# Kernel optimization log

Measured on AMD Instinct MI355X. Metric: run time of the kernel, lower is better.

The kernel has to match this reference:

```python
import jax, jax.numpy as jnp
import numpy as np

B, C, T, F = 4, 2, 4224, 256
L = 256          # sequence_len (block size over time)
STRIDE = 128
H = 8            # num_heads
RF = L // 2      # receptive_field default


def setup_inputs() -> dict:
    key = jax.random.key(0)
    k0, k1, k2, k3, k4 = jax.random.split(key, 5)
    s = 0.05
    return {
        "x": jax.random.normal(k0, (B, C, T, F), dtype=jnp.float32),
        "w_in": jax.random.normal(k1, (3 * F, F), dtype=jnp.float32) * s,
        "b_in": jax.random.normal(k2, (3 * F,), dtype=jnp.float32) * s,
        "w_out": jax.random.normal(k3, (F, F), dtype=jnp.float32) * s,
        "b_out": jax.random.normal(k4, (F,), dtype=jnp.float32) * s,
    }


def reference(x, w_in, b_in, w_out, b_out):
    b, c, t, f = x.shape
    nb = (t - L) // STRIDE + 1              # num_blocks
    dh = f // H                              # head dim

    # --- UnfoldSpectrogram: (B,C,T,F) -> (B,C,nb,L,F) ---
    idx = jnp.arange(nb)[:, None] * STRIDE + jnp.arange(L)[None, :]  # (nb, L)
    blocks = x[:, :, idx, :]                 # (B,C,nb,L,F)

    # --- MultiheadAttention over flattened batch of blocks ---
    xb = blocks.reshape(b * c * nb, L, f)    # (N,L,F)
    qkv = xb @ w_in.T + b_in                 # (N,L,3F)
    q, k, v = jnp.split(qkv, 3, axis=-1)
    q = q.reshape(-1, L, H, dh)
    k = k.reshape(-1, L, H, dh)
    v = v.reshape(-1, L, H, dh)

    scale = 1.0 / np.sqrt(dh).astype(np.float32)
    scores = jnp.einsum("nihd,njhd->nhij", q, k) * scale  # (N,H,L,L)

    # Faithful to the original: the Longformer mask is a FLOAT 0/1 tensor that
    # torch's MultiheadAttention ADDS to the scores (band gets +1.0).
    di = jnp.arange(L)[:, None] - jnp.arange(L)[None, :]
    band = ((di >= 0) & (di < RF)).astype(scores.dtype)   # (L,L)
    scores = scores + band

    attn = jax.nn.softmax(scores, axis=-1)
    o = jnp.einsum("nhij,njhd->nihd", attn, v).reshape(-1, L, f)
    o = o @ w_out.T + b_out                  # (N,L,F)

    # --- FoldSpectrogram: overlap-add then normalize by overlap count ---
    ob = o.reshape(b, c, nb, L, f)
    y = jnp.zeros((b, c, t, f), dtype=o.dtype).at[:, :, idx, :].add(ob)
    cnt = jnp.zeros((t,), dtype=o.dtype).at[idx.reshape(-1)].add(1.0)
    return y / cnt[None, None, :, None]
```

## Files before the change

### kernel.cpp

```cpp
#include <hip/hip_runtime.h>

typedef unsigned short u16;
typedef unsigned int u32;
typedef __attribute__((ext_vector_type(8))) short bf16x8;
typedef __attribute__((ext_vector_type(4))) float f32x4;
typedef __attribute__((ext_vector_type(4))) u32 u32x4;
typedef __attribute__((ext_vector_type(2))) u32 u32x2;

__device__ __forceinline__ u16 f2bf(float f) {
  u32 u = __builtin_bit_cast(u32, f);
  return (u16)((u + 0x7FFFu + ((u >> 16) & 1u)) >> 16);
}
__device__ __forceinline__ float bf2f(u16 b) {
  return __builtin_bit_cast(float, (u32)b << 16);
}

__device__ __forceinline__ float fexp2(float x) {
#if __has_builtin(__builtin_amdgcn_exp2f)
  return __builtin_amdgcn_exp2f(x);
#else
  return __expf(x * 0.6931471805599453f);
#endif
}

__device__ __forceinline__ void lds_async16(const void* g, void* l) {
  auto gp = reinterpret_cast<const __attribute__((address_space(1))) u32*>(
      reinterpret_cast<uintptr_t>(g));
  auto lp = reinterpret_cast<__attribute__((address_space(3))) u32*>(
      reinterpret_cast<uintptr_t>(l));
  __builtin_amdgcn_global_load_lds(gp, lp, 16, 0, 0);
}

__global__ void cvt_kernel(const float* __restrict__ in, u16* __restrict__ out, int n4) {
  int i = blockIdx.x * 256 + threadIdx.x;
  if (i < n4) {
    f32x4 v = *(const f32x4*)(in + (size_t)i * 4);
    u32x2 o;
    o[0] = (u32)f2bf(v[0]) | ((u32)f2bf(v[1]) << 16);
    o[1] = (u32)f2bf(v[2]) | ((u32)f2bf(v[3]) << 16);
    *(u32x2*)(out + (size_t)i * 4) = o;
  }
}

__global__ void cvt2_kernel(const float* __restrict__ a, const float* __restrict__ b,
                            u16* __restrict__ oa, u16* __restrict__ ob, int na4, int nb4) {
  int i = blockIdx.x * 256 + threadIdx.x;
  const float* src;
  u16* dst;
  int idx;
  if (i < na4) {
    src = a; dst = oa; idx = i;
  } else {
    idx = i - na4;
    if (idx >= nb4) return;
    src = b; dst = ob;
  }
  f32x4 v = *(const f32x4*)(src + (size_t)idx * 4);
  u32x2 o;
  o[0] = (u32)f2bf(v[0]) | ((u32)f2bf(v[1]) << 16);
  o[1] = (u32)f2bf(v[2]) | ((u32)f2bf(v[3]) << 16);
  *(u32x2*)(dst + (size_t)idx * 4) = o;
}

template <bool OUT_BF16>
__global__ __launch_bounds__(256) void gemm_bt_kernel(
    const u16* __restrict__ A, const u16* __restrict__ B,
    const float* __restrict__ bias, void* __restrict__ C,
    int M, int N, int K) {
  __shared__ u16 sA[128 * 32];
  __shared__ u16 sB[128 * 32];
  const int tid = threadIdx.x;
  const int m0 = blockIdx.x * 128;
  const int n0 = blockIdx.y * 128;
  const int w = tid >> 6;
  const int lane = tid & 63;
  const int wr = (w >> 1) * 64;
  const int wc = (w & 1) * 64;
  const int lm = lane & 15;
  const int lk = (lane >> 4) * 8;

  f32x4 acc[4][4] = {};

  const int srow = tid >> 2;
  const int ssub = (tid & 3) * 8;
  const u16* Ag = A + (size_t)(m0 + srow) * K + ssub;
  const u16* Bg = B + (size_t)(n0 + srow) * K + ssub;
  const size_t rstep = (size_t)64 * K;

  for (int k0 = 0; k0 < K; k0 += 32) {
    __syncthreads();
    lds_async16(Ag + k0, &sA[tid * 8]);
    lds_async16(Ag + rstep + k0, &sA[2048 + tid * 8]);
    lds_async16(Bg + k0, &sB[tid * 8]);
    lds_async16(Bg + rstep + k0, &sB[2048 + tid * 8]);
    __syncthreads();
    bf16x8 af[4], bfr[4];
#pragma unroll
    for (int i = 0; i < 4; ++i)
      af[i] = *(const bf16x8*)&sA[(wr + i * 16 + lm) * 32 + lk];
#pragma unroll
    for (int j = 0; j < 4; ++j)
      bfr[j] = *(const bf16x8*)&sB[(wc + j * 16 + lm) * 32 + lk];
#pragma unroll
    for (int i = 0; i < 4; ++i)
#pragma unroll
      for (int j = 0; j < 4; ++j)
        acc[i][j] = __builtin_amdgcn_mfma_f32_16x16x32_bf16(af[i], bfr[j], acc[i][j], 0, 0, 0);
  }

  const int r0 = (lane >> 4) * 4;
#pragma unroll
  for (int j = 0; j < 4; ++j) {
    const int n = n0 + wc + j * 16 + lm;
    const float bv = bias[n];
#pragma unroll
    for (int i = 0; i < 4; ++i) {
#pragma unroll
      for (int r = 0; r < 4; ++r) {
        const int m = m0 + wr + i * 16 + r0 + r;
        float v = acc[i][j][r] + bv;
        if (OUT_BF16)
          ((u16*)C)[(size_t)m * N + n] = f2bf(v);
        else
          ((float*)C)[(size_t)m * N + n] = v;
      }
    }
  }
}

__global__ __launch_bounds__(256, 2) void attn_kernel(const u16* __restrict__ qkv,
                                                      u16* __restrict__ o_ws) {
  __shared__ u16 sVt[32 * 264];
  __shared__ u16 sP[4 * 32 * 40];

  const int bid = blockIdx.x;
  const int n = bid >> 3;
  const int h = bid & 7;
  const int rowbase = (n >> 5) * 4224 + (n & 31) * 128;
  const int tid = threadIdx.x;
  const int w = tid >> 6;
  const int lane = tid & 63;
  const int lm = lane & 15;
  const int lg = lane >> 4;

#pragma unroll
  for (int it = 0; it < 4; ++it) {
    int c = it * 256 + tid;
    int row = c >> 2;
    int sub = (c & 3) * 8;
    const u16* gv = qkv + (size_t)(rowbase + row) * 768 + 512 + h * 32 + sub;
    u32x4 vv = *(const u32x4*)gv;
#pragma unroll
    for (int q = 0; q < 4; ++q) {
      sVt[(sub + 2 * q) * 264 + row] = (u16)(vv[q] & 0xFFFFu);
      sVt[(sub + 2 * q + 1) * 264 + row] = (u16)(vv[q] >> 16);
    }
  }

  bf16x8 qf[4];
#pragma unroll
  for (int rt = 0; rt < 4; ++rt) {
    int row = rowbase + w * 64 + rt * 16 + lm;
    qf[rt] = *(const bf16x8*)(qkv + (size_t)row * 768 + h * 32 + lg * 8);
  }

  __syncthreads();

  f32x4 oacc[4][2] = {};
  float lsum[4] = {0.f, 0.f, 0.f, 0.f};
  u16* myP = sP + w * (32 * 40);
  const float C1 = 0.25500035370494726f;
  const float C2 = 1.4426950408889634f;
  const int jq = lg * 4;
  const u16* kbase = qkv + (size_t)(rowbase + lm) * 768 + 256 + h * 32 + lg * 8;
  const int D0w = w * 64;

#pragma unroll 1
  for (int ch = 0; ch < 8; ++ch) {
    bf16x8 kf[2], vf[2];
#pragma unroll
    for (int ct = 0; ct < 2; ++ct)
      kf[ct] = *(const bf16x8*)(kbase + (size_t)(ch * 32 + ct * 16) * 768);
#pragma unroll
    for (int ctd = 0; ctd < 2; ++ctd)
      vf[ctd] = *(const bf16x8*)&sVt[(ctd * 16 + lm) * 264 + ch * 32 + lg * 8];

#pragma unroll
    for (int hf = 0; hf < 2; ++hf) {
#pragma unroll
      for (int ct = 0; ct < 2; ++ct) {
#pragma unroll
        for (int rl = 0; rl < 2; ++rl) {
          const int rt = hf * 2 + rl;
          f32x4 s = __builtin_amdgcn_mfma_f32_16x16x32_bf16(kf[ct], qf[rt], f32x4{0.f, 0.f, 0.f, 0.f}, 0, 0, 0);
          const int D0 = D0w + rt * 16 - (ch * 32 + ct * 16);
          float p0, p1, p2, p3;
          if (D0 >= 16 && D0 <= 112) {
            p0 = fexp2(__builtin_fmaf(s[0], C1, C2));
            p1 = fexp2(__builtin_fmaf(s[1], C1, C2));
            p2 = fexp2(__builtin_fmaf(s[2], C1, C2));
            p3 = fexp2(__builtin_fmaf(s[3], C1, C2));
          } else if (D0 == 0) {
            p0 = fexp2(__builtin_fmaf(s[0], C1, (lm >= jq + 0) ? C2 : 0.0f));
            p1 = fexp2(__builtin_fmaf(s[1], C1, (lm >= jq + 1) ? C2 : 0.0f));
            p2 = fexp2(__builtin_fmaf(s[2], C1, (lm >= jq + 2) ? C2 : 0.0f));
            p3 = fexp2(__builtin_fmaf(s[3], C1, (lm >= jq + 3) ? C2 : 0.0f));
          } else if (D0 == 128) {
            p0 = fexp2(__builtin_fmaf(s[0], C1, (lm < jq + 0) ? C2 : 0.0f));
            p1 = fexp2(__builtin_fmaf(s[1], C1, (lm < jq + 1) ? C2 : 0.0f));
            p2 = fexp2(__builtin_fmaf(s[2], C1, (lm < jq + 2) ? C2 : 0.0f));
            p3 = fexp2(__builtin_fmaf(s[3], C1, (lm < jq + 3) ? C2 : 0.0f));
          } else {
            p0 = fexp2(s[0] * C1);
            p1 = fexp2(s[1] * C1);
            p2 = fexp2(s[2] * C1);
            p3 = fexp2(s[3] * C1);
          }
          lsum[rt] += (p0 + p1) + (p2 + p3);
          u32 u0 = __builtin_bit_cast(u32, p0) + 0x8000u;
          u32 u1 = __builtin_bit_cast(u32, p1) + 0x8000u;
          u32 u2 = __builtin_bit_cast(u32, p2) + 0x8000u;
          u32 u3 = __builtin_bit_cast(u32, p3) + 0x8000u;
          u32x2 pk;
          pk[0] = __builtin_amdgcn_perm(u1, u0, 0x07060302u);
          pk[1] = __builtin_amdgcn_perm(u3, u2, 0x07060302u);
          *(u32x2*)&myP[(rl * 16 + lm) * 40 + ct * 16 + jq] = pk;
        }
      }
      bf16x8 pf[2];
#pragma unroll
      for (int rl = 0; rl < 2; ++rl)
        pf[rl] = *(const bf16x8*)&myP[(rl * 16 + lm) * 40 + lg * 8];
      __asm__ __volatile__("" ::: "memory");
#pragma unroll
      for (int rl = 0; rl < 2; ++rl)
#pragma unroll
        for (int ctd = 0; ctd < 2; ++ctd)
          oacc[hf * 2 + rl][ctd] =
              __builtin_amdgcn_mfma_f32_16x16x32_bf16(pf[rl], vf[ctd], oacc[hf * 2 + rl][ctd], 0, 0, 0);
    }
  }

  float linv[4];
#pragma unroll
  for (int rt = 0; rt < 4; ++rt) {
    float v = lsum[rt];
    v += __shfl_xor(v, 16);
    v += __shfl_xor(v, 32);
    linv[rt] = 1.0f / v;
  }

#pragma unroll
  for (int rt = 0; rt < 4; ++rt) {
#pragma unroll
    for (int r = 0; r < 4; ++r) {
      float inv = __shfl(linv[rt], jq + r);
      int i_g = w * 64 + rt * 16 + jq + r;
#pragma unroll
      for (int ctd = 0; ctd < 2; ++ctd) {
        float v = oacc[rt][ctd][r] * inv;
        u32 u = __builtin_bit_cast(u32, v) + 0x8000u;
        o_ws[((size_t)(n * 256 + i_g)) * 256 + h * 32 + ctd * 16 + lm] = (u16)(u >> 16);
      }
    }
  }
}

__global__ void combine_kernel(const u16* __restrict__ o_ws, u16* __restrict__ oc) {
  int gid = blockIdx.x * 256 + threadIdx.x;
  int m = gid >> 5;
  int f0 = (gid & 31) << 3;
  int bc = m / 4224;
  int t = m - bc * 4224;
  int i0 = t >> 7;
  float a[8] = {0.f, 0.f, 0.f, 0.f, 0.f, 0.f, 0.f, 0.f};
  if (i0 <= 31) {
    const u16* p = o_ws + ((size_t)((bc * 32 + i0) * 256 + (t - (i0 << 7)))) * 256 + f0;
    u32x4 v = *(const u32x4*)p;
#pragma unroll
    for (int q = 0; q < 4; ++q) {
      a[2 * q] += bf2f((u16)(v[q] & 0xFFFFu));
      a[2 * q + 1] += bf2f((u16)(v[q] >> 16));
    }
  }
  if (i0 >= 1) {
    int i1 = i0 - 1;
    const u16* p = o_ws + ((size_t)((bc * 32 + i1) * 256 + (t - (i1 << 7)))) * 256 + f0;
    u32x4 v = *(const u32x4*)p;
#pragma unroll
    for (int q = 0; q < 4; ++q) {
      a[2 * q] += bf2f((u16)(v[q] & 0xFFFFu));
      a[2 * q + 1] += bf2f((u16)(v[q] >> 16));
    }
  }
  float sc = (i0 >= 1 && i0 <= 31) ? 0.5f : 1.0f;
  u32x2 o;
  o[0] = (u32)f2bf(a[0] * sc) | ((u32)f2bf(a[1] * sc) << 16);
  o[1] = (u32)f2bf(a[2] * sc) | ((u32)f2bf(a[3] * sc) << 16);
  u32x2 o2;
  o2[0] = (u32)f2bf(a[4] * sc) | ((u32)f2bf(a[5] * sc) << 16);
  o2[1] = (u32)f2bf(a[6] * sc) | ((u32)f2bf(a[7] * sc) << 16);
  u16* dst = oc + (size_t)m * 256 + f0;
  *(u32x2*)dst = o;
  *(u32x2*)(dst + 4) = o2;
}

extern "C" void kernel_launch(void* const* d_in, const int* in_sizes, int n_in,
                              void* d_out, int out_size, void* d_ws, size_t ws_size,
                              hipStream_t stream) {
  const float* x = (const float*)d_in[0];
  const float* w_in = (const float*)d_in[1];
  const float* b_in = (const float*)d_in[2];
  const float* w_out = (const float*)d_in[3];
  const float* b_out = (const float*)d_in[4];
  float* y = (float*)d_out;
  char* ws = (char*)d_ws;

  u16* qkv = (u16*)(ws);
  u16* xbf = (u16*)(ws + 51904512);
  u16* ows = (u16*)(ws + 69206016);
  u16* winb = (u16*)(ws + 102760448);
  u16* woutb = (u16*)(ws + 103153664);

  cvt_kernel<<<8448, 256, 0, stream>>>(x, xbf, 2162688);
  cvt2_kernel<<<256, 256, 0, stream>>>(w_in, w_out, winb, woutb, 49152, 16384);

  gemm_bt_kernel<true><<<dim3(264, 6), 256, 0, stream>>>(xbf, winb, b_in, qkv, 33792, 768, 256);

  attn_kernel<<<2048, 256, 0, stream>>>(qkv, ows);

  combine_kernel<<<4224, 256, 0, stream>>>(ows, xbf);

  gemm_bt_kernel<false><<<dim3(264, 2), 256, 0, stream>>>(xbf, woutb, b_out, y, 33792, 256, 256);
}
```

Before: 185.4 us.

## Fuse input conversion and overlap-add combine into the projection GEMMs

Result: no change. 187.2 us (+1.0%).

```diff
diff --git a/kernel.cpp b/kernel.cpp
--- a/kernel.cpp
+++ b/kernel.cpp
@@ -14,6 +14,13 @@
 __device__ __forceinline__ float bf2f(u16 b) {
   return __builtin_bit_cast(float, (u32)b << 16);
 }
+__device__ __forceinline__ u32 packbf2(float x, float y) {
+  u32 ux = __builtin_bit_cast(u32, x);
+  ux += 0x7FFFu + ((ux >> 16) & 1u);
+  u32 uy = __builtin_bit_cast(u32, y);
+  uy += 0x7FFFu + ((uy >> 16) & 1u);
+  return __builtin_amdgcn_perm(uy, ux, 0x07060302u);
+}
 
 __device__ __forceinline__ float fexp2(float x) {
 #if __has_builtin(__builtin_amdgcn_exp2f)
@@ -29,17 +36,6 @@
   auto lp = reinterpret_cast<__attribute__((address_space(3))) u32*>(
       reinterpret_cast<uintptr_t>(l));
   __builtin_amdgcn_global_load_lds(gp, lp, 16, 0, 0);
-}
-
-__global__ void cvt_kernel(const float* __restrict__ in, u16* __restrict__ out, int n4) {
-  int i = blockIdx.x * 256 + threadIdx.x;
-  if (i < n4) {
-    f32x4 v = *(const f32x4*)(in + (size_t)i * 4);
-    u32x2 o;
-    o[0] = (u32)f2bf(v[0]) | ((u32)f2bf(v[1]) << 16);
-    o[1] = (u32)f2bf(v[2]) | ((u32)f2bf(v[3]) << 16);
-    *(u32x2*)(out + (size_t)i * 4) = o;
-  }
 }
 
 __global__ void cvt2_kernel(const float* __restrict__ a, const float* __restrict__ b,
@@ -57,21 +53,21 @@
   }
   f32x4 v = *(const f32x4*)(src + (size_t)idx * 4);
   u32x2 o;
-  o[0] = (u32)f2bf(v[0]) | ((u32)f2bf(v[1]) << 16);
-  o[1] = (u32)f2bf(v[2]) | ((u32)f2bf(v[3]) << 16);
+  o[0] = packbf2(v[0], v[1]);
+  o[1] = packbf2(v[2], v[3]);
   *(u32x2*)(dst + (size_t)idx * 4) = o;
 }
 
-template <bool OUT_BF16>
-__global__ __launch_bounds__(256) void gemm_bt_kernel(
-    const u16* __restrict__ A, const u16* __restrict__ B,
-    const float* __restrict__ bias, void* __restrict__ C,
-    int M, int N, int K) {
+__global__ __launch_bounds__(256) void gemm_qkv_kernel(
+    const float* __restrict__ X, const u16* __restrict__ B,
+    const float* __restrict__ bias, u16* __restrict__ C) {
+  const int N = 768, K = 256;
   __shared__ u16 sA[128 * 32];
   __shared__ u16 sB[128 * 32];
   const int tid = threadIdx.x;
-  const int m0 = blockIdx.x * 128;
-  const int n0 = blockIdx.y * 128;
+  const int bid = blockIdx.x;
+  const int m0 = (bid / 6) * 128;
+  const int n0 = (bid % 6) * 128;
   const int w = tid >> 6;
   const int lane = tid & 63;
   const int wr = (w >> 1) * 64;
@@ -83,16 +79,28 @@
 
   const int srow = tid >> 2;
   const int ssub = (tid & 3) * 8;
-  const u16* Ag = A + (size_t)(m0 + srow) * K + ssub;
+  const float* Ag0 = X + (size_t)(m0 + srow) * K + ssub;
+  const float* Ag1 = Ag0 + (size_t)64 * K;
   const u16* Bg = B + (size_t)(n0 + srow) * K + ssub;
   const size_t rstep = (size_t)64 * K;
 
   for (int k0 = 0; k0 < K; k0 += 32) {
     __syncthreads();
-    lds_async16(Ag + k0, &sA[tid * 8]);
-    lds_async16(Ag + rstep + k0, &sA[2048 + tid * 8]);
     lds_async16(Bg + k0, &sB[tid * 8]);
     lds_async16(Bg + rstep + k0, &sB[2048 + tid * 8]);
+    {
+      f32x4 a0 = *(const f32x4*)(Ag0 + k0);
+      f32x4 a1 = *(const f32x4*)(Ag0 + k0 + 4);
+      f32x4 c0 = *(const f32x4*)(Ag1 + k0);
+      f32x4 c1 = *(const f32x4*)(Ag1 + k0 + 4);
+      u32x4 pa, pc;
+      pa[0] = packbf2(a0[0], a0[1]); pa[1] = packbf2(a0[2], a0[3]);
+      pa[2] = packbf2(a1[0], a1[1]); pa[3] = packbf2(a1[2], a1[3]);
+      pc[0] = packbf2(c0[0], c0[1]); pc[1] = packbf2(c0[2], c0[3]);
+      pc[2] = packbf2(c1[0], c1[1]); pc[3] = packbf2(c1[2], c1[3]);
+      *(u32x4*)&sA[tid * 8] = pa;
+      *(u32x4*)&sA[2048 + tid * 8] = pc;
+    }
     __syncthreads();
     bf16x8 af[4], bfr[4];
 #pragma unroll
@@ -118,11 +126,92 @@
 #pragma unroll
       for (int r = 0; r < 4; ++r) {
         const int m = m0 + wr + i * 16 + r0 + r;
-        float v = acc[i][j][r] + bv;
-        if (OUT_BF16)
-          ((u16*)C)[(size_t)m * N + n] = f2bf(v);
-        else
-          ((float*)C)[(size_t)m * N + n] = v;
+        C[(size_t)m * N + n] = f2bf(acc[i][j][r] + bv);
+      }
+    }
+  }
+}
+
+__global__ __launch_bounds__(256) void gemm_out_kernel(
+    const u16* __restrict__ OWS, const u16* __restrict__ B,
+    const float* __restrict__ bias, float* __restrict__ C) {
+  const int N = 256, K = 256;
+  __shared__ u16 sA[128 * 32];
+  __shared__ u16 sB[128 * 32];
+  const int tid = threadIdx.x;
+  const int bid = blockIdx.x;
+  const int m0 = (bid >> 1) * 128;
+  const int n0 = (bid & 1) * 128;
+  const int w = tid >> 6;
+  const int lane = tid & 63;
+  const int wr = (w >> 1) * 64;
+  const int wc = (w & 1) * 64;
+  const int lm = lane & 15;
+  const int lk = (lane >> 4) * 8;
+
+  f32x4 acc[4][4] = {};
+
+  const int srow = tid >> 2;
+  const int ssub = (tid & 3) * 8;
+  const u16* Bg = B + (size_t)(n0 + srow) * K + ssub;
+  const size_t rstep = (size_t)64 * K;
+
+  const u16* p[2][2];
+#pragma unroll
+  for (int hh = 0; hh < 2; ++hh) {
+    int m = m0 + hh * 64 + srow;
+    int bc = m / 4224;
+    int t = m - bc * 4224;
+    int i0 = t >> 7;
+    const u16* q0 = OWS + (((size_t)((bc * 32 + i0) * 256 + (t - (i0 << 7)))) << 8) + ssub;
+    const u16* q1 = OWS + (((size_t)((bc * 32 + (i0 - 1)) * 256 + (t - ((i0 - 1) << 7)))) << 8) + ssub;
+    p[hh][0] = (i0 <= 31) ? q0 : q1;
+    p[hh][1] = (i0 >= 1) ? q1 : q0;
+  }
+
+  for (int k0 = 0; k0 < K; k0 += 32) {
+    __syncthreads();
+    lds_async16(Bg + k0, &sB[tid * 8]);
+    lds_async16(Bg + rstep + k0, &sB[2048 + tid * 8]);
+#pragma unroll
+    for (int hh = 0; hh < 2; ++hh) {
+      u32x4 v0 = *(const u32x4*)(p[hh][0] + k0);
+      u32x4 v1 = *(const u32x4*)(p[hh][1] + k0);
+      u32x4 o;
+#pragma unroll
+      for (int q = 0; q < 4; ++q) {
+        float a0 = bf2f((u16)(v0[q] & 0xFFFFu)), b0 = bf2f((u16)(v1[q] & 0xFFFFu));
+        float a1 = bf2f((u16)(v0[q] >> 16)),     b1 = bf2f((u16)(v1[q] >> 16));
+        o[q] = packbf2((a0 + b0) * 0.5f, (a1 + b1) * 0.5f);
+      }
+      *(u32x4*)&sA[hh * 2048 + tid * 8] = o;
+    }
+    __syncthreads();
+    bf16x8 af[4], bfr[4];
+#pragma unroll
+    for (int i = 0; i < 4; ++i)
+      af[i] = *(const bf16x8*)&sA[(wr + i * 16 + lm) * 32 + lk];
+#pragma unroll
+    for (int j = 0; j < 4; ++j)
+      bfr[j] = *(const bf16x8*)&sB[(wc + j * 16 + lm) * 32 + lk];
+#pragma unroll
+    for (int i = 0; i < 4; ++i)
+#pragma unroll
+      for (int j = 0; j < 4; ++j)
+        acc[i][j] = __builtin_amdgcn_mfma_f32_16x16x32_bf16(af[i], bfr[j], acc[i][j], 0, 0, 0);
+  }
+
+  const int r0 = (lane >> 4) * 4;
+#pragma unroll
+  for (int j = 0; j < 4; ++j) {
+    const int n = n0 + wc + j * 16 + lm;
+    const float bv = bias[n];
+#pragma unroll
+    for (int i = 0; i < 4; ++i) {
+#pragma unroll
+      for (int r = 0; r < 4; ++r) {
+        const int m = m0 + wr + i * 16 + r0 + r;
+        C[(size_t)m * N + n] = acc[i][j][r] + bv;
       }
     }
   }
@@ -266,45 +355,6 @@
   }
 }
 
-__global__ void combine_kernel(const u16* __restrict__ o_ws, u16* __restrict__ oc) {
-  int gid = blockIdx.x * 256 + threadIdx.x;
-  int m = gid >> 5;
-  int f0 = (gid & 31) << 3;
-  int bc = m / 4224;
-  int t = m - bc * 4224;
-  int i0 = t >> 7;
-  float a[8] = {0.f, 0.f, 0.f, 0.f, 0.f, 0.f, 0.f, 0.f};
-  if (i0 <= 31) {
-    const u16* p = o_ws + ((size_t)((bc * 32 + i0) * 256 + (t - (i0 << 7)))) * 256 + f0;
-    u32x4 v = *(const u32x4*)p;
-#pragma unroll
-    for (int q = 0; q < 4; ++q) {
-      a[2 * q] += bf2f((u16)(v[q] & 0xFFFFu));
-      a[2 * q + 1] += bf2f((u16)(v[q] >> 16));
-    }
-  }
-  if (i0 >= 1) {
-    int i1 = i0 - 1;
-    const u16* p = o_ws + ((size_t)((bc * 32 + i1) * 256 + (t - (i1 << 7)))) * 256 + f0;
-    u32x4 v = *(const u32x4*)p;
-#pragma unroll
-    for (int q = 0; q < 4; ++q) {
-      a[2 * q] += bf2f((u16)(v[q] & 0xFFFFu));
-      a[2 * q + 1] += bf2f((u16)(v[q] >> 16));
-    }
-  }
-  float sc = (i0 >= 1 && i0 <= 31) ? 0.5f : 1.0f;
-  u32x2 o;
-  o[0] = (u32)f2bf(a[0] * sc) | ((u32)f2bf(a[1] * sc) << 16);
-  o[1] = (u32)f2bf(a[2] * sc) | ((u32)f2bf(a[3] * sc) << 16);
-  u32x2 o2;
-  o2[0] = (u32)f2bf(a[4] * sc) | ((u32)f2bf(a[5] * sc) << 16);
-  o2[1] = (u32)f2bf(a[6] * sc) | ((u32)f2bf(a[7] * sc) << 16);
-  u16* dst = oc + (size_t)m * 256 + f0;
-  *(u32x2*)dst = o;
-  *(u32x2*)(dst + 4) = o2;
-}
-
 extern "C" void kernel_launch(void* const* d_in, const int* in_sizes, int n_in,
                               void* d_out, int out_size, void* d_ws, size_t ws_size,
                               hipStream_t stream) {
@@ -317,19 +367,15 @@
   char* ws = (char*)d_ws;
 
   u16* qkv = (u16*)(ws);
-  u16* xbf = (u16*)(ws + 51904512);
-  u16* ows = (u16*)(ws + 69206016);
-  u16* winb = (u16*)(ws + 102760448);
-  u16* woutb = (u16*)(ws + 103153664);
-
-  cvt_kernel<<<8448, 256, 0, stream>>>(x, xbf, 2162688);
+  u16* ows = (u16*)(ws + 51904512);
+  u16* winb = (u16*)(ws + 85458944);
+  u16* woutb = (u16*)(ws + 85852160);
+
   cvt2_kernel<<<256, 256, 0, stream>>>(w_in, w_out, winb, woutb, 49152, 16384);
 
-  gemm_bt_kernel<true><<<dim3(264, 6), 256, 0, stream>>>(xbf, winb, b_in, qkv, 33792, 768, 256);
+  gemm_qkv_kernel<<<1584, 256, 0, stream>>>(x, winb, b_in, qkv);
 
   attn_kernel<<<2048, 256, 0, stream>>>(qkv, ows);
 
-  combine_kernel<<<4224, 256, 0, stream>>>(ows, xbf);
-
-  gemm_bt_kernel<false><<<dim3(264, 2), 256, 0, stream>>>(xbf, woutb, b_out, y, 33792, 256, 256);
-}
+  gemm_out_kernel<<<528, 256, 0, stream>>>(ows, woutb, b_out, y);
+}
```
